# Optimization experiments

Measured on AMD Instinct MI355X. Metric: run time of the kernel, lower is better.

Reference implementation:

```python
import jax, jax.numpy as jnp
import numpy as np
import math

VOCAB = 32000; D = 256; H = 8; HD = D // H; S = 2048; MLP = 1024; NC = 2
B = 4; L = 4; VEC = 8; M = S // VEC; MMA_K = 16; SPARSITY = 0.9


def _pos_encoding():
    pos = jnp.arange(S, dtype=jnp.float32)[:, None]
    div = jnp.exp(jnp.arange(0, D, 2, dtype=jnp.float32) * (-math.log(10000.0) / D))
    ang = pos * div  # [S, D//2]
    # interleave sin (even dims) / cos (odd dims)
    return jnp.stack([jnp.sin(ang), jnp.cos(ang)], axis=-1).reshape(S, D)


def _ln(x, g, b):
    mu = x.mean(-1, keepdims=True)
    var = x.var(-1, keepdims=True)
    return (x - mu) / jnp.sqrt(var + 1e-5) * g + b


def setup_inputs() -> dict:
    rng = np.random.default_rng(0)
    # nnz per block-row, aligned to mma_k_dim as in static_random_mask_aligned
    nnz = max(MMA_K, int(S * (1.0 - SPARSITY)) // MMA_K * MMA_K)
    mask = np.zeros((L, M, S), dtype=bool)
    for l in range(L):
        idx = np.argsort(rng.random((M, S)), axis=1)[:, :nnz]
        np.put_along_axis(mask[l], idx, True, axis=1)
    k = jax.random.key(0)
    ks = jax.random.split(k, 8)
    f = jnp.float32
    w = lambda key, shape, s=0.02: jax.random.normal(key, shape, dtype=f) * s
    return dict(
        x=jax.random.randint(ks[0], (B, S), 0, VOCAB),
        mask=jnp.asarray(mask),
        emb=w(ks[1], (VOCAB, D), 1.0),
        ln1_g=jnp.ones((L, D), f), ln1_b=jnp.zeros((L, D), f),
        in_w=w(ks[2], (L, 3 * D, D)), in_b=jnp.zeros((L, 3 * D), f),
        out_w=w(ks[3], (L, D, D)), out_b=jnp.zeros((L, D), f),
        ln2_g=jnp.ones((L, D), f), ln2_b=jnp.zeros((L, D), f),
        w1=w(ks[4], (L, MLP, D)), b1=jnp.zeros((L, MLP), f),
        w2=w(ks[5], (L, D, MLP)), b2=jnp.zeros((L, D), f),
        lnf_g=jnp.ones((D,), f), lnf_b=jnp.zeros((D,), f),
        wf=w(ks[6], (NC, D)), bf=jnp.zeros((NC,), f),
    )


def reference(x, mask, emb, ln1_g, ln1_b, in_w, in_b, out_w, out_b,
              ln2_g, ln2_b, w1, b1, w2, b2, lnf_g, lnf_b, wf, bf):
    h = emb[x] * jnp.sqrt(jnp.float32(D))          # [B,S,D]
    h = jnp.transpose(h, (1, 0, 2)) + _pos_encoding()[:, None, :]  # [S,B,D]
    neg = jnp.finfo(jnp.float32).min
    scale = 1.0 / jnp.sqrt(jnp.float32(HD))
    for l in range(L):
        # expand block-row mask: each of M rows covers VEC consecutive queries
        mfull = jnp.repeat(mask[l], VEC, axis=0)   # [S,S]
        o = _ln(h, ln1_g[l], ln1_b[l])
        qkv = o @ in_w[l].T + in_b[l]              # [S,B,3D]
        q, kk, v = [t.reshape(S, B, H, HD) for t in jnp.split(qkv, 3, axis=-1)]
        scores = jnp.einsum('sbhd,tbhd->bhst', q * scale, kk)
        scores = jnp.where(mfull[None, None], scores, neg)
        att = jax.nn.softmax(scores, axis=-1)
        ao = jnp.einsum('bhst,tbhd->sbhd', att, v).reshape(S, B, D)
        h2 = ao @ out_w[l].T + out_b[l] + h        # attn residual (block input)
        o2 = _ln(h2, ln2_g[l], ln2_b[l])
        ff = (o2 @ w1[l].T + b1[l]) @ w2[l].T + b2[l]  # note: no activation, per source
        h = ff + h                                  # final residual uses BLOCK INPUT, per source
    o = _ln(h, lnf_g, lnf_b)
    return o @ wf.T + bf                            # [S,B,NC]
```

## Files before the change

kernel.cpp:

```cpp
#include <hip/hip_runtime.h>
#include <hip/hip_bf16.h>
#include <math.h>

#define D_ 256
#define S_ 2048
#define B_ 4
#define H_ 8
#define HD_ 32
#define MLP_ 1024
#define L_ 4
#define M_ 256
#define NNZ 192
#define ROWS 8192

typedef __attribute__((ext_vector_type(8))) short bf16x8;
typedef __attribute__((ext_vector_type(8))) unsigned short u16x8;
typedef __attribute__((ext_vector_type(4))) float f32x4;
typedef __attribute__((ext_vector_type(4))) int i32x4;

__device__ __forceinline__ unsigned short f2bf(float f) {
    union { float f; unsigned u; } c; c.f = f;
    unsigned r = (c.u + 0x7FFFu + ((c.u >> 16) & 1u)) >> 16;
    return (unsigned short)r;
}
__device__ __forceinline__ float bf2f(unsigned short u) {
    union { unsigned u; float f; } c; c.u = (unsigned)u << 16;
    return c.f;
}

__global__ __launch_bounds__(256) void detect_mask_kernel(const unsigned int* __restrict__ mask,
                                                          int* __restrict__ flag) {
    int i = blockIdx.x * 256 + threadIdx.x;
    uint4 v = *(const uint4*)&mask[i * 4];
    bool hit = ((v.x | v.y | v.z | v.w) & 0x0000FF00u) != 0;
    if (__ballot(hit)) {
        if ((threadIdx.x & 63) == 0) atomicOr(flag, 1);
        else if (hit) atomicOr(flag, 1);
    }
}

__global__ __launch_bounds__(256) void build_idx_kernel(const void* __restrict__ mask,
                                                        int* __restrict__ idx,
                                                        const int* __restrict__ flagp) {
    int wave = threadIdx.x >> 6, lane = threadIdx.x & 63;
    int row = blockIdx.x * 4 + wave;
    int isbyte = *flagp;
    const unsigned char* mb = (const unsigned char*)mask;
    const int* mi = (const int*)mask;
    int base = 0;
    for (int c = 0; c < S_ / 64; c++) {
        int t = c * 64 + lane;
        size_t off = (size_t)row * S_ + t;
        bool bit = isbyte ? (mb[off] != 0) : (mi[off] != 0);
        unsigned long long bm = __ballot(bit);
        if (bit) {
            int pos = base + __popcll(bm & ((1ull << lane) - 1ull));
            if (pos < NNZ) idx[row * NNZ + pos] = t;
        }
        base += __popcll(bm);
    }
}

__global__ __launch_bounds__(256) void cvt_all_kernel(const float* __restrict__ in_w,
                                                      const float* __restrict__ out_w,
                                                      const float* __restrict__ w1,
                                                      const float* __restrict__ w2,
                                                      unsigned short* __restrict__ in_w_bf,
                                                      unsigned short* __restrict__ out_w_bf,
                                                      unsigned short* __restrict__ w1_bf,
                                                      unsigned short* __restrict__ w2_bf) {
    int i = blockIdx.x * 256 + threadIdx.x;
    const float* src; unsigned short* dst; int off;
    if (i < 196608)      { src = in_w;  dst = in_w_bf;  off = i; }
    else if (i < 262144) { src = out_w; dst = out_w_bf; off = i - 196608; }
    else if (i < 524288) { src = w1;    dst = w1_bf;    off = i - 262144; }
    else                 { src = w2;    dst = w2_bf;    off = i - 524288; }
    float4 v = *(const float4*)&src[(size_t)off * 4];
    ushort4 o;
    o.x = f2bf(v.x); o.y = f2bf(v.y); o.z = f2bf(v.z); o.w = f2bf(v.w);
    *(ushort4*)&dst[(size_t)off * 4] = o;
}

__global__ __launch_bounds__(256) void embed_kernel(const int* __restrict__ x,
                                                    const float* __restrict__ emb,
                                                    float* __restrict__ h) {
    int e = blockIdx.x * 256 + threadIdx.x;
    int r = e >> 7, i = e & 127;
    int s = r >> 2, b = r & 3;
    int tok = x[b * S_ + s];
    float div = expf(-(float)(2 * i) * (9.210340371976184f / 256.0f));
    float ang = (float)s * div;
    float sv = sinf(ang), cv = cosf(ang);
    float2 ev = *(const float2*)&emb[(size_t)tok * D_ + 2 * i];
    float2 hv;
    hv.x = ev.x * 16.0f + sv;
    hv.y = ev.y * 16.0f + cv;
    *(float2*)&h[(size_t)r * D_ + 2 * i] = hv;
}

__global__ __launch_bounds__(256) void ln_kernel(const float* __restrict__ x,
                                                 const float* __restrict__ g,
                                                 const float* __restrict__ b,
                                                 unsigned short* __restrict__ o) {
    int row = blockIdx.x * 4 + (threadIdx.x >> 6);
    int lane = threadIdx.x & 63;
    float4 v = *(const float4*)&x[(size_t)row * D_ + lane * 4];
    float s = v.x + v.y + v.z + v.w;
    float ss = v.x * v.x + v.y * v.y + v.z * v.z + v.w * v.w;
#pragma unroll
    for (int off = 32; off; off >>= 1) {
        s += __shfl_xor(s, off, 64);
        ss += __shfl_xor(ss, off, 64);
    }
    float mu = s * (1.0f / 256.0f);
    float var = ss * (1.0f / 256.0f) - mu * mu;
    float rstd = rsqrtf(var + 1e-5f);
    float4 gv = *(const float4*)&g[lane * 4];
    float4 bv = *(const float4*)&b[lane * 4];
    ushort4 ov;
    ov.x = f2bf((v.x - mu) * rstd * gv.x + bv.x);
    ov.y = f2bf((v.y - mu) * rstd * gv.y + bv.y);
    ov.z = f2bf((v.z - mu) * rstd * gv.z + bv.z);
    ov.w = f2bf((v.w - mu) * rstd * gv.w + bv.w);
    *(ushort4*)&o[(size_t)row * D_ + lane * 4] = ov;
}

#define BM 128
#define BN 64
#define BK 32
#define PK 40

template<int OUT_BF16>
__global__ __launch_bounds__(256) void gemm_bf16_nt(const unsigned short* __restrict__ A,
                                                    const unsigned short* __restrict__ W,
                                                    const float* __restrict__ bias,
                                                    const float* __restrict__ res,
                                                    void* __restrict__ Cp,
                                                    int N, int K) {
    __shared__ unsigned short As[BM * PK];
    __shared__ unsigned short Ws[BN * PK];
    int tid = threadIdx.x;
    int m0 = blockIdx.y * BM, n0 = blockIdx.x * BN;
    int w = tid >> 6, l = tid & 63;
    int wr = (w >> 1) * 64, wc = (w & 1) * 32;

    f32x4 acc[4][2];
#pragma unroll
    for (int mi = 0; mi < 4; mi++)
#pragma unroll
        for (int ni = 0; ni < 2; ni++) acc[mi][ni] = (f32x4){0.f, 0.f, 0.f, 0.f};

    int arow = tid >> 1, ak = (tid & 1) * 16;
    int wrow = tid >> 2, wk = (tid & 3) * 8;
    const unsigned short* Ag = &A[(size_t)(m0 + arow) * K + ak];
    const unsigned short* Wg = &W[(size_t)(n0 + wrow) * K + wk];

    int rl = l & 15, koff = (l >> 4) * 8;

    for (int kt = 0; kt < K; kt += BK) {
        i32x4 a0 = *(const i32x4*)(Ag + kt);
        i32x4 a1 = *(const i32x4*)(Ag + kt + 8);
        i32x4 w0 = *(const i32x4*)(Wg + kt);
        __syncthreads();
        *(i32x4*)&As[arow * PK + ak] = a0;
        *(i32x4*)&As[arow * PK + ak + 8] = a1;
        *(i32x4*)&Ws[wrow * PK + wk] = w0;
        __syncthreads();
        bf16x8 af[4], wf[2];
#pragma unroll
        for (int mi = 0; mi < 4; mi++)
            af[mi] = *(const bf16x8*)&As[(wr + mi * 16 + rl) * PK + koff];
#pragma unroll
        for (int ni = 0; ni < 2; ni++)
            wf[ni] = *(const bf16x8*)&Ws[(wc + ni * 16 + rl) * PK + koff];
#pragma unroll
        for (int mi = 0; mi < 4; mi++)
#pragma unroll
            for (int ni = 0; ni < 2; ni++)
                acc[mi][ni] = __builtin_amdgcn_mfma_f32_16x16x32_bf16(af[mi], wf[ni], acc[mi][ni], 0, 0, 0);
    }

    int col = l & 15, rbase = (l >> 4) * 4;
#pragma unroll
    for (int mi = 0; mi < 4; mi++) {
#pragma unroll
        for (int ni = 0; ni < 2; ni++) {
            int c = n0 + wc + ni * 16 + col;
            float bv = bias[c];
#pragma unroll
            for (int j = 0; j < 4; j++) {
                int r = m0 + wr + mi * 16 + rbase + j;
                float v = acc[mi][ni][j] + bv;
                if (res) v += res[(size_t)r * N + c];
                if (OUT_BF16) ((unsigned short*)Cp)[(size_t)r * N + c] = f2bf(v);
                else ((float*)Cp)[(size_t)r * N + c] = v;
            }
        }
    }
}

#define KST 40
#define VST 200

__global__ __launch_bounds__(256, 4) void attn_kernel(const unsigned short* __restrict__ qkv,
                                                      const int* __restrict__ idx,
                                                      unsigned short* __restrict__ ao) {
    __shared__ int cols[NNZ];
    __shared__ unsigned short Kt[NNZ * KST];
    __shared__ unsigned short Vt[HD_ * VST];
    __shared__ unsigned short Pl[8 * VST];
    __shared__ float mpart[4][8];
    __shared__ float spart[4][8];

    int blk = blockIdx.x;
    int m = blk & 255, hh = (blk >> 8) & 7, b = blk >> 11;
    int tid = threadIdx.x;
    int w = tid >> 6;
    int gg = (tid >> 4) & 3;
    int rl = tid & 15;

    if (tid < NNZ) cols[tid] = idx[m * NNZ + tid];
    __syncthreads();

#pragma unroll
    for (int k = 0; k < 3; k++) {
        int e = tid + 256 * k;
        int j = e % NNZ;
        int c = e / NNZ;
        size_t base = ((size_t)(cols[j] * 4 + b)) * 768 + hh * HD_ + c * 8;
        i32x4 kv = *(const i32x4*)&qkv[base + 256];
        *(i32x4*)&Kt[j * KST + c * 8] = kv;
        u16x8 vv = *(const u16x8*)&qkv[base + 512];
#pragma unroll
        for (int i2 = 0; i2 < 8; i2++)
            Vt[(c * 8 + i2) * VST + j] = vv[i2];
    }
    bf16x8 afq;
    if (rl < 8) {
        size_t qa = ((size_t)((m * 8 + rl) * 4 + b)) * 768 + hh * HD_ + gg * 8;
        afq = *(const bf16x8*)&qkv[qa];
    } else {
        afq = (bf16x8){0, 0, 0, 0, 0, 0, 0, 0};
    }
    __syncthreads();

    f32x4 acc[3];
#pragma unroll
    for (int t = 0; t < 3; t++) {
        int jt = w * 3 + t;
        bf16x8 bk = *(const bf16x8*)&Kt[(jt * 16 + rl) * KST + gg * 8];
        acc[t] = __builtin_amdgcn_mfma_f32_16x16x32_bf16(afq, bk,
                   (f32x4){0.f, 0.f, 0.f, 0.f}, 0, 0, 0);
    }

    float mv[4];
#pragma unroll
    for (int r = 0; r < 4; r++) {
        float mx = fmaxf(fmaxf(acc[0][r], acc[1][r]), acc[2][r]);
#pragma unroll
        for (int off = 1; off <= 8; off <<= 1) mx = fmaxf(mx, __shfl_xor(mx, off, 64));
        mv[r] = mx;
    }
    if (rl == 0 && gg < 2) {
#pragma unroll
        for (int r = 0; r < 4; r++) mpart[w][gg * 4 + r] = mv[r];
    }
    __syncthreads();
    int qbase = (gg & 1) * 4;
    float mx[4], ev[3][4], sv[4];
#pragma unroll
    for (int r = 0; r < 4; r++) {
        float a = fmaxf(fmaxf(mpart[0][qbase + r], mpart[1][qbase + r]),
                        fmaxf(mpart[2][qbase + r], mpart[3][qbase + r]));
        mx[r] = a;
        float s = 0.f;
#pragma unroll
        for (int t = 0; t < 3; t++) {
            ev[t][r] = __expf((acc[t][r] - a) * 0.17677669529663687f);
            s += ev[t][r];
        }
#pragma unroll
        for (int off = 1; off <= 8; off <<= 1) s += __shfl_xor(s, off, 64);
        sv[r] = s;
    }
    if (rl == 0 && gg < 2) {
#pragma unroll
        for (int r = 0; r < 4; r++) spart[w][gg * 4 + r] = sv[r];
    }
    __syncthreads();
    if (gg < 2) {
#pragma unroll
        for (int r = 0; r < 4; r++) {
            float inv = 1.0f / (spart[0][qbase + r] + spart[1][qbase + r] +
                                spart[2][qbase + r] + spart[3][qbase + r]);
            int q = gg * 4 + r;
#pragma unroll
            for (int t = 0; t < 3; t++)
                Pl[q * VST + (w * 3 + t) * 16 + rl] = f2bf(ev[t][r] * inv);
        }
    }
    __syncthreads();

    if (w < 2) {
        f32x4 oacc = (f32x4){0.f, 0.f, 0.f, 0.f};
#pragma unroll
        for (int ks = 0; ks < 6; ks++) {
            bf16x8 ap = *(const bf16x8*)&Pl[(rl & 7) * VST + ks * 32 + gg * 8];
            bf16x8 bv = *(const bf16x8*)&Vt[(w * 16 + rl) * VST + ks * 32 + gg * 8];
            oacc = __builtin_amdgcn_mfma_f32_16x16x32_bf16(ap, bv, oacc, 0, 0, 0);
        }
        if (gg < 2) {
#pragma unroll
            for (int r = 0; r < 4; r++) {
                int q = gg * 4 + r;
                size_t oa = ((size_t)((m * 8 + q) * 4 + b)) * 256 + hh * HD_ + w * 16 + rl;
                ao[oa] = f2bf(oacc[r]);
            }
        }
    }
}

__global__ __launch_bounds__(256) void final_kernel(const float* __restrict__ h,
                                                    const float* __restrict__ g,
                                                    const float* __restrict__ b,
                                                    const float* __restrict__ wf,
                                                    const float* __restrict__ bf,
                                                    float* __restrict__ out) {
    int row = blockIdx.x * 4 + (threadIdx.x >> 6);
    int lane = threadIdx.x & 63;
    float4 v = *(const float4*)&h[(size_t)row * D_ + lane * 4];
    float s = v.x + v.y + v.z + v.w;
    float ss = v.x * v.x + v.y * v.y + v.z * v.z + v.w * v.w;
#pragma unroll
    for (int off = 32; off; off >>= 1) {
        s += __shfl_xor(s, off, 64);
        ss += __shfl_xor(ss, off, 64);
    }
    float mu = s * (1.0f / 256.0f);
    float var = ss * (1.0f / 256.0f) - mu * mu;
    float rstd = rsqrtf(var + 1e-5f);
    float4 gv = *(const float4*)&g[lane * 4];
    float4 bv = *(const float4*)&b[lane * 4];
    float o0 = (v.x - mu) * rstd * gv.x + bv.x;
    float o1 = (v.y - mu) * rstd * gv.y + bv.y;
    float o2 = (v.z - mu) * rstd * gv.z + bv.z;
    float o3 = (v.w - mu) * rstd * gv.w + bv.w;
    float4 w0 = *(const float4*)&wf[lane * 4];
    float4 w1 = *(const float4*)&wf[D_ + lane * 4];
    float a0 = o0 * w0.x + o1 * w0.y + o2 * w0.z + o3 * w0.w;
    float a1 = o0 * w1.x + o1 * w1.y + o2 * w1.z + o3 * w1.w;
#pragma unroll
    for (int off = 32; off; off >>= 1) {
        a0 += __shfl_xor(a0, off, 64);
        a1 += __shfl_xor(a1, off, 64);
    }
    if (lane == 0) {
        out[(size_t)row * 2 + 0] = a0 + bf[0];
        out[(size_t)row * 2 + 1] = a1 + bf[1];
    }
}

extern "C" void kernel_launch(void* const* d_in, const int* in_sizes, int n_in,
                              void* d_out, int out_size, void* d_ws, size_t ws_size,
                              hipStream_t stream) {
    const int* x = (const int*)d_in[0];
    const void* mask = d_in[1];
    const float* emb = (const float*)d_in[2];
    const float* ln1_g = (const float*)d_in[3];
    const float* ln1_b = (const float*)d_in[4];
    const float* in_w = (const float*)d_in[5];
    const float* in_b = (const float*)d_in[6];
    const float* out_w = (const float*)d_in[7];
    const float* out_b = (const float*)d_in[8];
    const float* ln2_g = (const float*)d_in[9];
    const float* ln2_b = (const float*)d_in[10];
    const float* w1 = (const float*)d_in[11];
    const float* b1 = (const float*)d_in[12];
    const float* w2 = (const float*)d_in[13];
    const float* b2 = (const float*)d_in[14];
    const float* lnf_g = (const float*)d_in[15];
    const float* lnf_b = (const float*)d_in[16];
    const float* wf = (const float*)d_in[17];
    const float* bfp = (const float*)d_in[18];
    float* out = (float*)d_out;

    const size_t MB = 1024 * 1024;
    char* ws = (char*)d_ws;
    int* idx = (int*)ws;
    int* flag = (int*)(ws + 786432);
    float* h = (float*)(ws + 1 * MB);
    unsigned short* o = (unsigned short*)(ws + 9 * MB);
    unsigned short* ao = o;
    float* h2 = (float*)(ws + 13 * MB);
    unsigned short* qkvb = (unsigned short*)(ws + 21 * MB);
    unsigned short* ff1 = (unsigned short*)(ws + 21 * MB);
    unsigned short* wbf = (unsigned short*)(ws + 37 * MB);
    unsigned short* in_w_bf = wbf;
    unsigned short* out_w_bf = wbf + 786432;
    unsigned short* w1_bf = wbf + 1048576;
    unsigned short* w2_bf = wbf + 2097152;

    hipMemsetAsync(flag, 0, sizeof(int), stream);
    detect_mask_kernel<<<16, 256, 0, stream>>>((const unsigned int*)mask, flag);
    build_idx_kernel<<<L_ * M_ / 4, 256, 0, stream>>>(mask, idx, flag);
    cvt_all_kernel<<<3072, 256, 0, stream>>>(in_w, out_w, w1, w2,
                                             in_w_bf, out_w_bf, w1_bf, w2_bf);
    embed_kernel<<<ROWS * (D_ / 2) / 256, 256, 0, stream>>>(x, emb, h);

    for (int l = 0; l < L_; l++) {
        ln_kernel<<<ROWS / 4, 256, 0, stream>>>(h, ln1_g + l * D_, ln1_b + l * D_, o);
        gemm_bf16_nt<1><<<dim3(768 / BN, ROWS / BM), 256, 0, stream>>>(
            o, in_w_bf + (size_t)l * 768 * D_, in_b + l * 768, nullptr, qkvb, 768, D_);
        attn_kernel<<<B_ * H_ * M_, 256, 0, stream>>>(qkvb, idx + l * M_ * NNZ, ao);
        gemm_bf16_nt<0><<<dim3(D_ / BN, ROWS / BM), 256, 0, stream>>>(
            ao, out_w_bf + (size_t)l * D_ * D_, out_b + l * D_, h, h2, D_, D_);
        ln_kernel<<<ROWS / 4, 256, 0, stream>>>(h2, ln2_g + l * D_, ln2_b + l * D_, o);
        gemm_bf16_nt<1><<<dim3(MLP_ / BN, ROWS / BM), 256, 0, stream>>>(
            o, w1_bf + (size_t)l * MLP_ * D_, b1 + l * MLP_, nullptr, ff1, MLP_, D_);
        gemm_bf16_nt<0><<<dim3(D_ / BN, ROWS / BM), 256, 0, stream>>>(
            ff1, w2_bf + (size_t)l * D_ * MLP_, b2 + l * D_, h, h, D_, MLP_);
    }
    final_kernel<<<ROWS / 4, 256, 0, stream>>>(h, lnf_g, lnf_b, wf, bfp, out);
}
```

Baseline: 650.6 us.

## Use direct global-to-LDS loads and 128x128 tiles in bf16 GEMM

```diff
diff --git a/kernel.cpp b/kernel.cpp
--- a/kernel.cpp
+++ b/kernel.cpp
@@ -27,6 +27,10 @@
     union { unsigned u; float f; } c; c.u = (unsigned)u << 16;
     return c.f;
 }
+
+#define GLOAD16(gsrc, ldst) __builtin_amdgcn_global_load_lds( \
+    (const __attribute__((address_space(1))) unsigned int*)(gsrc), \
+    (__attribute__((address_space(3))) unsigned int*)(ldst), 16, 0, 0)
 
 __global__ __launch_bounds__(256) void detect_mask_kernel(const unsigned int* __restrict__ mask,
                                                           int* __restrict__ flag) {
@@ -125,71 +129,67 @@
     *(ushort4*)&o[(size_t)row * D_ + lane * 4] = ov;
 }
 
-#define BM 128
-#define BN 64
-#define BK 32
-#define PK 40
+#define GBM 128
+#define GBN 128
+#define GBK 32
 
 template<int OUT_BF16>
-__global__ __launch_bounds__(256) void gemm_bf16_nt(const unsigned short* __restrict__ A,
+__global__ __launch_bounds__(256) void gemm_bf16_v2(const unsigned short* __restrict__ A,
                                                     const unsigned short* __restrict__ W,
                                                     const float* __restrict__ bias,
                                                     const float* __restrict__ res,
                                                     void* __restrict__ Cp,
                                                     int N, int K) {
-    __shared__ unsigned short As[BM * PK];
-    __shared__ unsigned short Ws[BN * PK];
+    __shared__ unsigned short As[GBM * GBK];
+    __shared__ unsigned short Ws[GBN * GBK];
     int tid = threadIdx.x;
-    int m0 = blockIdx.y * BM, n0 = blockIdx.x * BN;
+    int m0 = blockIdx.y * GBM, n0 = blockIdx.x * GBN;
     int w = tid >> 6, l = tid & 63;
-    int wr = (w >> 1) * 64, wc = (w & 1) * 32;
-
-    f32x4 acc[4][2];
+    int wr = (w >> 1) * 64, wc = (w & 1) * 64;
+    int rl = l & 15, koff = (l >> 4) * 8;
+
+    f32x4 acc[4][4];
 #pragma unroll
     for (int mi = 0; mi < 4; mi++)
 #pragma unroll
-        for (int ni = 0; ni < 2; ni++) acc[mi][ni] = (f32x4){0.f, 0.f, 0.f, 0.f};
-
-    int arow = tid >> 1, ak = (tid & 1) * 16;
-    int wrow = tid >> 2, wk = (tid & 3) * 8;
-    const unsigned short* Ag = &A[(size_t)(m0 + arow) * K + ak];
-    const unsigned short* Wg = &W[(size_t)(n0 + wrow) * K + wk];
-
-    int rl = l & 15, koff = (l >> 4) * 8;
-
-    for (int kt = 0; kt < K; kt += BK) {
-        i32x4 a0 = *(const i32x4*)(Ag + kt);
-        i32x4 a1 = *(const i32x4*)(Ag + kt + 8);
-        i32x4 w0 = *(const i32x4*)(Wg + kt);
+        for (int ni = 0; ni < 4; ni++) acc[mi][ni] = (f32x4){0.f, 0.f, 0.f, 0.f};
+
+    int crow = l >> 2;
+    int cgr = (l & 3) * 8;
+
+    for (int kt = 0; kt < K; kt += GBK) {
         __syncthreads();
-        *(i32x4*)&As[arow * PK + ak] = a0;
-        *(i32x4*)&As[arow * PK + ak + 8] = a1;
-        *(i32x4*)&Ws[wrow * PK + wk] = w0;
+#pragma unroll
+        for (int c = 0; c < 2; c++) {
+            int rbase = (w * 2 + c) * 16;
+            GLOAD16(&A[(size_t)(m0 + rbase + crow) * K + kt + cgr], &As[rbase * GBK]);
+            GLOAD16(&W[(size_t)(n0 + rbase + crow) * K + kt + cgr], &Ws[rbase * GBK]);
+        }
         __syncthreads();
-        bf16x8 af[4], wf[2];
+        bf16x8 af[4], wf[4];
 #pragma unroll
         for (int mi = 0; mi < 4; mi++)
-            af[mi] = *(const bf16x8*)&As[(wr + mi * 16 + rl) * PK + koff];
-#pragma unroll
-        for (int ni = 0; ni < 2; ni++)
-            wf[ni] = *(const bf16x8*)&Ws[(wc + ni * 16 + rl) * PK + koff];
+            af[mi] = *(const bf16x8*)&As[(wr + mi * 16 + rl) * GBK + koff];
+#pragma unroll
+        for (int ni = 0; ni < 4; ni++)
+            wf[ni] = *(const bf16x8*)&Ws[(wc + ni * 16 + rl) * GBK + koff];
 #pragma unroll
         for (int mi = 0; mi < 4; mi++)
 #pragma unroll
-            for (int ni = 0; ni < 2; ni++)
+            for (int ni = 0; ni < 4; ni++)
                 acc[mi][ni] = __builtin_amdgcn_mfma_f32_16x16x32_bf16(af[mi], wf[ni], acc[mi][ni], 0, 0, 0);
     }
 
-    int col = l & 15, rbase = (l >> 4) * 4;
+    int col = l & 15, rbase2 = (l >> 4) * 4;
 #pragma unroll
     for (int mi = 0; mi < 4; mi++) {
 #pragma unroll
-        for (int ni = 0; ni < 2; ni++) {
+        for (int ni = 0; ni < 4; ni++) {
             int c = n0 + wc + ni * 16 + col;
             float bv = bias[c];
 #pragma unroll
             for (int j = 0; j < 4; j++) {
-                int r = m0 + wr + mi * 16 + rbase + j;
+                int r = m0 + wr + mi * 16 + rbase2 + j;
                 float v = acc[mi][ni][j] + bv;
                 if (res) v += res[(size_t)r * N + c];
                 if (OUT_BF16) ((unsigned short*)Cp)[(size_t)r * N + c] = f2bf(v);
@@ -267,12 +267,11 @@
     }
     __syncthreads();
     int qbase = (gg & 1) * 4;
-    float mx[4], ev[3][4], sv[4];
+    float ev[3][4], sv[4];
 #pragma unroll
     for (int r = 0; r < 4; r++) {
         float a = fmaxf(fmaxf(mpart[0][qbase + r], mpart[1][qbase + r]),
                         fmaxf(mpart[2][qbase + r], mpart[3][qbase + r]));
-        mx[r] = a;
         float s = 0.f;
 #pragma unroll
         for (int t = 0; t < 3; t++) {
@@ -409,15 +408,15 @@
 
     for (int l = 0; l < L_; l++) {
         ln_kernel<<<ROWS / 4, 256, 0, stream>>>(h, ln1_g + l * D_, ln1_b + l * D_, o);
-        gemm_bf16_nt<1><<<dim3(768 / BN, ROWS / BM), 256, 0, stream>>>(
+        gemm_bf16_v2<1><<<dim3(768 / GBN, ROWS / GBM), 256, 0, stream>>>(
             o, in_w_bf + (size_t)l * 768 * D_, in_b + l * 768, nullptr, qkvb, 768, D_);
         attn_kernel<<<B_ * H_ * M_, 256, 0, stream>>>(qkvb, idx + l * M_ * NNZ, ao);
-        gemm_bf16_nt<0><<<dim3(D_ / BN, ROWS / BM), 256, 0, stream>>>(
+        gemm_bf16_v2<0><<<dim3(D_ / GBN, ROWS / GBM), 256, 0, stream>>>(
             ao, out_w_bf + (size_t)l * D_ * D_, out_b + l * D_, h, h2, D_, D_);
         ln_kernel<<<ROWS / 4, 256, 0, stream>>>(h2, ln2_g + l * D_, ln2_b + l * D_, o);
-        gemm_bf16_nt<1><<<dim3(MLP_ / BN, ROWS / BM), 256, 0, stream>>>(
+        gemm_bf16_v2<1><<<dim3(MLP_ / GBN, ROWS / GBM), 256, 0, stream>>>(
             o, w1_bf + (size_t)l * MLP_ * D_, b1 + l * MLP_, nullptr, ff1, MLP_, D_);
-        gemm_bf16_nt<0><<<dim3(D_ / BN, ROWS / BM), 256, 0, stream>>>(
+        gemm_bf16_v2<0><<<dim3(D_ / GBN, ROWS / GBM), 256, 0, stream>>>(
             ff1, w2_bf + (size_t)l * D_ * MLP_, b2 + l * D_, h, h, D_, MLP_);
     }
     final_kernel<<<ROWS / 4, 256, 0, stream>>>(h, lnf_g, lnf_b, wf, bfp, out);
```

After: 722.7 us. +11.1%, slower.
